# Performance work log

Hardware: AMD Instinct MI355X
Metric: run time of the kernel (lower is better)

Reference implementation:

```python
import jax, jax.numpy as jnp
import numpy as np

BN_SCALE = np.float32(1.0 / np.sqrt(1.0 + 1e-5))  # eval-mode BatchNorm: (x-0)/sqrt(1+eps)

_SPECS = {
    'x': (128, 4096, 64),
    'e_w1': (64, 64, 7),  'e_b1': (64,),
    'e_w2': (128, 64, 5), 'e_b2': (128,),
    'e_w3': (256, 128, 3),'e_b3': (256,),
    'e_w5': (256, 256, 4),'e_b5': (256,),
    'd_w1': (64, 64, 7),  'd_b1': (64,),
    'd_w2': (128, 64, 5), 'd_b2': (128,),
    'd_w3': (256, 128, 3),'d_b3': (256,),
    'd_w5': (256, 256, 4),'d_b5': (256,),
    'e_wih': (1024, 256), 'e_whh': (1024, 256), 'e_bih': (1024,), 'e_bhh': (1024,),
    'd_wih': (1024, 512), 'd_whh': (1024, 256), 'd_bih': (1024,), 'd_bhh': (1024,),
    'a_w1': (256, 512), 'a_b1': (256,), 'a_w2': (1, 256), 'a_b2': (1,),
    'f_w1': (16, 256), 'f_b1': (16,), 'f_w2': (8, 16), 'f_b2': (8,),
}

def setup_inputs() -> dict:
    key = jax.random.key(0)
    ks = jax.random.split(key, len(_SPECS))
    out = {}
    for k, (name, shape) in zip(ks, _SPECS.items()):
        scale = 1.0 if name == 'x' else 0.05
        out[name] = jax.random.normal(k, shape, dtype=jnp.float32) * scale
    return out

def _conv1d(x, w, b, pad):
    # x: (B,C,L), w: (O,I,K)
    y = jax.lax.conv_general_dilated(x, w, window_strides=(1,), padding=[(pad, pad)],
                                     dimension_numbers=('NCH', 'OIH', 'NCH'))
    return y + b[None, :, None]

def _maxpool(x, k):
    return jax.lax.reduce_window(x, -jnp.inf, jax.lax.max, (1, 1, k), (1, 1, k), 'VALID')

def _convnet(x, p):
    # faithful to the source: torch.reshape (raw reshape, NOT transpose)
    B, S, D = x.shape
    x = x.reshape(B, D, S)
    x = jax.nn.relu(_maxpool(_conv1d(x, p[0], p[1], 2), 4) * BN_SCALE)
    x = jax.nn.relu(_maxpool(_conv1d(x, p[2], p[3], 2), 4) * BN_SCALE)
    x = jax.nn.relu(_maxpool(_conv1d(x, p[4], p[5], 2), 2) * BN_SCALE)
    x = _conv1d(x, p[6], p[7], 2)
    B, C, L = x.shape
    return x.reshape(B, L, C)  # raw reshape, as in source

def _lstm_step(hs, cs, xt, wih, whh, bih, bhh):
    g = xt @ wih.T + bih + hs @ whh.T + bhh
    i, f, gg, o = jnp.split(g, 4, axis=-1)
    cs = jax.nn.sigmoid(f) * cs + jax.nn.sigmoid(i) * jnp.tanh(gg)
    hs = jax.nn.sigmoid(o) * jnp.tanh(cs)
    return hs, cs

def _forward(x, e_w1, e_b1, e_w2, e_b2, e_w3, e_b3, e_w5, e_b5,
             d_w1, d_b1, d_w2, d_b2, d_w3, d_b3, d_w5, d_b5,
             e_wih, e_whh, e_bih, e_bhh, d_wih, d_whh, d_bih, d_bhh,
             a_w1, a_b1, a_w2, a_b2, f_w1, f_b1, f_w2, f_b2):
    B = x.shape[0]
    H = e_whh.shape[1]
    enc = _convnet(x, (e_w1, e_b1, e_w2, e_b2, e_w3, e_b3, e_w5, e_b5))  # (B,T,4D)
    h0 = jnp.zeros((B, H), x.dtype)
    c0 = jnp.zeros((B, H), x.dtype)

    def enc_step(carry, xt):
        hs, cs = _lstm_step(carry[0], carry[1], xt, e_wih, e_whh, e_bih, e_bhh)
        return (hs, cs), hs
    (hs, cs), ann = jax.lax.scan(enc_step, (h0, c0), jnp.swapaxes(enc, 0, 1))
    ann = jnp.swapaxes(ann, 0, 1)  # (B,T,H)

    dec = _convnet(x, (d_w1, d_b1, d_w2, d_b2, d_w3, d_b3, d_w5, d_b5))  # (B,T,4D)

    def dec_step(carry, xt):
        hs, cs = carry
        q = jnp.broadcast_to(hs[:, None, :], ann.shape)          # (B,T,H)
        cat = jnp.concatenate([q, ann], axis=2)                  # (B,T,2H)
        u = jax.nn.relu(jnp.einsum('btk,hk->bth', cat, a_w1) + a_b1)
        u = jnp.einsum('bth,oh->bto', u, a_w2) + a_b2            # (B,T,1)
        w = jax.nn.softmax(u, axis=1)
        ctx = jnp.einsum('bto,bth->bh', w, ann)                  # (B,H)
        inp = jnp.concatenate([xt, ctx], axis=1)                 # (B,4D+H)
        hs, cs = _lstm_step(hs, cs, inp, d_wih, d_whh, d_bih, d_bhh)
        return (hs, cs), None
    (hs, cs), _ = jax.lax.scan(dec_step, (hs, cs), jnp.swapaxes(dec, 0, 1))

    y = jax.nn.relu(hs @ f_w1.T + f_b1)
    return jax.nn.sigmoid(y @ f_w2.T + f_b2)

def reference(x, e_w1, e_b1, e_w2, e_b2, e_w3, e_b3, e_w5, e_b5,
              d_w1, d_b1, d_w2, d_b2, d_w3, d_b3, d_w5, d_b5,
              e_wih, e_whh, e_bih, e_bhh, d_wih, d_whh, d_bih, d_bhh,
              a_w1, a_b1, a_w2, a_b2, f_w1, f_b1, f_w2, f_b2):
    return _forward(x, e_w1, e_b1, e_w2, e_b2, e_w3, e_b3, e_w5, e_b5,
                    d_w1, d_b1, d_w2, d_b2, d_w3, d_b3, d_w5, d_b5,
                    e_wih, e_whh, e_bih, e_bhh, d_wih, d_whh, d_bih, d_bhh,
                    a_w1, a_b1, a_w2, a_b2, f_w1, f_b1, f_w2, f_b2)
```

## Files before the change

kernel.cpp:

```cpp
#include <hip/hip_runtime.h>
#include <cmath>

#define BN_SCALE 0.9999950000374997f

__device__ __forceinline__ float sigm(float x) { return 1.f / (1.f + __expf(-x)); }

__device__ __forceinline__ void gsync(unsigned* bar, unsigned target) {
    __syncthreads();
    if (threadIdx.x == 0) {
        __threadfence();
        atomicAdd(bar, 1u);
        while (__hip_atomic_load(bar, __ATOMIC_RELAXED, __HIP_MEMORY_SCOPE_AGENT) < target)
            __builtin_amdgcn_s_sleep(2);
        __threadfence();
    }
    __syncthreads();
}

template<int I, int K, int POOL, int O4, int OPAR, int IC, bool ACT>
__global__ __launch_bounds__(256) void conv2k(
    const float* __restrict__ in, const float* __restrict__ w,
    const float* __restrict__ bias, float* __restrict__ out,
    int O, int Lin, int Lpool)
{
    constexpr int TLP = 256 / OPAR;
    constexpr int NLP = TLP * 4;
    constexpr int LC  = NLP / POOL;
    constexpr int SEG = NLP + K - 1;
    constexpr int PW  = O4 * OPAR;
    constexpr int ICH = I / IC;
    __shared__ float xs[IC * SEG];
    __shared__ float ws[PW * IC * K];

    const int chunk = blockIdx.x, b = blockIdx.y, tid = threadIdx.x;
    const int l0 = chunk * LC;
    const int jbase = chunk * NLP - 2;
    const int tlp = tid % TLP, og = tid / TLP;
    const int lp0 = tlp * 4;
    const int npass = O / PW;
    const float* inb = in + (size_t)b * I * Lin;

    for (int p = 0; p < npass; ++p) {
        float acc[O4][4];
        #pragma unroll
        for (int oo = 0; oo < O4; ++oo)
            #pragma unroll
            for (int j = 0; j < 4; ++j) acc[oo][j] = 0.f;

        for (int c = 0; c < ICH; ++c) {
            __syncthreads();
            for (int idx = tid; idx < PW * IC * K; idx += 256) {
                int oo = idx / (IC * K); int rem = idx % (IC * K);
                int ii = rem / K; int k = rem % K;
                ws[idx] = w[(size_t)((p * PW + oo) * I + c * IC + ii) * K + k];
            }
            if (ICH > 1 || p == 0) {
                for (int idx = tid; idx < IC * SEG; idx += 256) {
                    int ii = idx / SEG, s = idx % SEG;
                    int j = jbase + s;
                    float v = 0.f;
                    if (j >= 0 && j < Lin) v = inb[(size_t)(c * IC + ii) * Lin + j];
                    xs[idx] = v;
                }
            }
            __syncthreads();
            for (int ii = 0; ii < IC; ++ii) {
                float xv[K + 3];
                #pragma unroll
                for (int k = 0; k < K + 3; ++k) xv[k] = xs[ii * SEG + lp0 + k];
                #pragma unroll
                for (int oo = 0; oo < O4; ++oo) {
                    const float* wr = &ws[((og * O4 + oo) * IC + ii) * K];
                    #pragma unroll
                    for (int k = 0; k < K; ++k) {
                        float wv = wr[k];
                        acc[oo][0] += wv * xv[k];
                        acc[oo][1] += wv * xv[k + 1];
                        acc[oo][2] += wv * xv[k + 2];
                        acc[oo][3] += wv * xv[k + 3];
                    }
                }
            }
        }
        #pragma unroll
        for (int oo = 0; oo < O4; ++oo) {
            int o = p * PW + og * O4 + oo;
            float bv = bias[o];
            #pragma unroll
            for (int wnd = 0; wnd < 4 / POOL; ++wnd) {
                float m = acc[oo][wnd * POOL];
                #pragma unroll
                for (int q = 1; q < POOL; ++q) m = fmaxf(m, acc[oo][wnd * POOL + q]);
                int l = l0 + lp0 / POOL + wnd;
                if (l < Lpool) {
                    float v = m + bv;
                    if (ACT) v = fmaxf(v * BN_SCALE, 0.f);
                    out[((size_t)b * O + o) * Lpool + l] = v;
                }
            }
        }
    }
}

__global__ __launch_bounds__(256) void transpose_kt(
    const float* __restrict__ in, float* __restrict__ out, int N, int ldin, int off)
{
    int idx = blockIdx.x * 256 + threadIdx.x;
    int k = idx / N, n = idx % N;
    out[idx] = in[(size_t)n * ldin + off + k];
}

__global__ __launch_bounds__(256) void pack_aw1hs(
    const float* __restrict__ aw1, float* __restrict__ out)
{
    int idx = blockIdx.x * 256 + threadIdx.x;
    int c = idx & 3, h = (idx >> 2) & 255, k4 = idx >> 10;
    out[idx] = aw1[(size_t)h * 512 + k4 * 4 + c];
}

template<int N>
__global__ __launch_bounds__(256) void gemm16(
    const float* __restrict__ X, const float* __restrict__ WT,
    const float* __restrict__ b1, const float* __restrict__ b2,
    float* __restrict__ OUT, int outT, int outB)
{
    constexpr int NL = N / 4;
    constexpr int MS = N >> 6;
    __shared__ float xsh[16][257];
    const int m0 = blockIdx.x * 16;
    const int tt = m0 >> 7, bb0 = m0 & 127;
    const int tid = threadIdx.x;
    for (int it = 0; it < 16; ++it)
        xsh[it][tid] = X[(size_t)(bb0 + it) * 33024 + tt * 256 + tid];
    __syncthreads();
    const int mg = tid / NL, nl = tid % NL;
    float4 acc[MS];
    #pragma unroll
    for (int i = 0; i < MS; ++i) acc[i] = make_float4(0.f, 0.f, 0.f, 0.f);
    for (int k = 0; k < 256; ++k) {
        float4 wv = *(const float4*)(WT + (size_t)k * N + nl * 4);
        #pragma unroll
        for (int ms = 0; ms < MS; ++ms) {
            float s = xsh[mg * MS + ms][k];
            acc[ms].x += wv.x * s; acc[ms].y += wv.y * s;
            acc[ms].z += wv.z * s; acc[ms].w += wv.w * s;
        }
    }
    float4 bv = *(const float4*)(b1 + nl * 4);
    if (b2) {
        float4 b2v = *(const float4*)(b2 + nl * 4);
        bv.x += b2v.x; bv.y += b2v.y; bv.z += b2v.z; bv.w += b2v.w;
    }
    #pragma unroll
    for (int ms = 0; ms < MS; ++ms) {
        int mi = mg * MS + ms;
        float4 v = acc[ms];
        v.x += bv.x; v.y += bv.y; v.z += bv.z; v.w += bv.w;
        *(float4*)(OUT + (size_t)tt * outT + (size_t)(bb0 + mi) * outB + nl * 4) = v;
    }
}

__global__ __launch_bounds__(256) void enc_persist(
    const float* __restrict__ IH, const float* __restrict__ whh,
    float* __restrict__ hs0, float* __restrict__ hs1,
    float* __restrict__ cs_out, float* __restrict__ ann, unsigned* __restrict__ bar)
{
    const int blk = blockIdx.x, tid = threadIdx.x;
    const int jg = blk & 31, bg = blk >> 5;
    __shared__ float whh_sl[32 * 260];
    __shared__ float hs_l[16 * 260];
    __shared__ float g_l[16 * 33];
    for (int r = 0; r < 32; ++r) {
        int o = (r >> 3) * 256 + jg * 8 + (r & 7);
        whh_sl[r * 260 + tid] = whh[(size_t)o * 256 + tid];
    }
    float cs_r = 0.f;
    unsigned phase = 0;
    __syncthreads();
    for (int step = 0; step < 129; ++step) {
        const float* cur = (step & 1) ? hs1 : hs0;
        float* nxt = (step & 1) ? hs0 : hs1;
        for (int it = 0; it < 16; ++it)
            hs_l[it * 260 + tid] = cur[(bg * 16 + it) * 256 + tid];
        __syncthreads();
        const int bb = tid >> 4, r0 = tid & 15;
        #pragma unroll
        for (int half = 0; half < 2; ++half) {
            int r = r0 + half * 16;
            int o = (r >> 3) * 256 + jg * 8 + (r & 7);
            float a = IH[(size_t)step * 131072 + (size_t)(bg * 16 + bb) * 1024 + o];
            const float* wr = &whh_sl[r * 260];
            const float* hr = &hs_l[bb * 260];
            for (int k4 = 0; k4 < 64; ++k4) {
                float4 w4 = *(const float4*)(wr + k4 * 4);
                float4 h4 = *(const float4*)(hr + k4 * 4);
                a += w4.x * h4.x + w4.y * h4.y + w4.z * h4.z + w4.w * h4.w;
            }
            g_l[bb * 33 + r] = a;
        }
        __syncthreads();
        if (tid < 128) {
            int bb2 = tid >> 3, jj = tid & 7;
            float gi = g_l[bb2 * 33 + jj],      gf = g_l[bb2 * 33 + 8 + jj];
            float gg = g_l[bb2 * 33 + 16 + jj], go = g_l[bb2 * 33 + 24 + jj];
            float cn = sigm(gf) * cs_r + sigm(gi) * tanhf(gg);
            float hn = sigm(go) * tanhf(cn);
            cs_r = cn;
            int b = bg * 16 + bb2, j = jg * 8 + jj;
            nxt[b * 256 + j] = hn;
            ann[(size_t)b * 33024 + step * 256 + j] = hn;
            if (step == 128) cs_out[b * 256 + j] = cn;
        }
        gsync(bar, 256u * (++phase));
    }
}

__global__ __launch_bounds__(256) void dec_persist(
    const float* __restrict__ IH, const float* __restrict__ dwih,
    const float* __restrict__ dwhh, const float* __restrict__ awhs4,
    const float* __restrict__ aw2, const float* __restrict__ ann,
    const float* __restrict__ annW, float* __restrict__ ctx_g,
    float* __restrict__ hs0, float* __restrict__ hs1,
    const float* __restrict__ cs_in, unsigned* __restrict__ bar)
{
    const int blk = blockIdx.x, tid = threadIdx.x;
    const int jg = blk & 31, bg = blk >> 5;
    __shared__ float wih_sl[32 * 260];
    __shared__ float whh_sl[32 * 260];
    __shared__ float hs_l[16 * 260];
    __shared__ float ctx_l[16 * 260];
    __shared__ float g_l[16 * 33];
    __shared__ float hs_a[256], hsW_l[256], aw2_l[256], evs[256], red[256];

    for (int r = 0; r < 32; ++r) {
        int o = (r >> 3) * 256 + jg * 8 + (r & 7);
        wih_sl[r * 260 + tid] = dwih[(size_t)o * 512 + 256 + tid];
        whh_sl[r * 260 + tid] = dwhh[(size_t)o * 256 + tid];
    }
    aw2_l[tid] = aw2[tid];
    float cs_r = 0.f;
    if (tid < 128)
        cs_r = cs_in[(size_t)(bg * 16 + (tid >> 3)) * 256 + jg * 8 + (tid & 7)];
    unsigned phase = 0;
    __syncthreads();

    for (int step = 0; step < 129; ++step) {
        const float* cur = (step & 1) ? hs1 : hs0;
        float* nxt = (step & 1) ? hs0 : hs1;
        if (blk < 128) {
            hs_a[tid] = cur[blk * 256 + tid];
            __syncthreads();
            float a = 0.f;
            for (int k4 = 0; k4 < 64; ++k4) {
                float4 wv = *(const float4*)(awhs4 + (size_t)k4 * 1024 + tid * 4);
                float4 hv = *(const float4*)(&hs_a[k4 * 4]);
                a += wv.x * hv.x + wv.y * hv.y + wv.z * hv.z + wv.w * hv.w;
            }
            hsW_l[tid] = a;
            __syncthreads();
            float sv = -3.0e38f;
            if (tid < 129) {
                const float* ar = annW + (size_t)blk * 33024 + tid * 256;
                float s = 0.f;
                for (int h4 = 0; h4 < 64; ++h4) {
                    float4 av = *(const float4*)(ar + h4 * 4);
                    s += fmaxf(hsW_l[h4*4+0] + av.x, 0.f) * aw2_l[h4*4+0];
                    s += fmaxf(hsW_l[h4*4+1] + av.y, 0.f) * aw2_l[h4*4+1];
                    s += fmaxf(hsW_l[h4*4+2] + av.z, 0.f) * aw2_l[h4*4+2];
                    s += fmaxf(hsW_l[h4*4+3] + av.w, 0.f) * aw2_l[h4*4+3];
                }
                sv = s;
            }
            red[tid] = sv; __syncthreads();
            for (int s2 = 128; s2 > 0; s2 >>= 1) {
                if (tid < s2) red[tid] = fmaxf(red[tid], red[tid + s2]);
                __syncthreads();
            }
            float mx = red[0]; __syncthreads();
            float e = (tid < 129) ? __expf(sv - mx) : 0.f;
            evs[tid] = e; red[tid] = e; __syncthreads();
            for (int s2 = 128; s2 > 0; s2 >>= 1) {
                if (tid < s2) red[tid] += red[tid + s2];
                __syncthreads();
            }
            float inv = 1.f / red[0];
            float c = 0.f;
            const float* ab = ann + (size_t)blk * 33024 + tid;
            for (int t2 = 0; t2 < 129; ++t2) c += evs[t2] * ab[(size_t)t2 * 256];
            ctx_g[blk * 256 + tid] = c * inv;
        }
        gsync(bar, 256u * (++phase));
        for (int it = 0; it < 16; ++it) {
            hs_l[it * 260 + tid]  = cur[(bg * 16 + it) * 256 + tid];
            ctx_l[it * 260 + tid] = ctx_g[(bg * 16 + it) * 256 + tid];
        }
        __syncthreads();
        {
            const int bb = tid >> 4, r0 = tid & 15;
            const float* hr = &hs_l[bb * 260];
            const float* cr = &ctx_l[bb * 260];
            #pragma unroll
            for (int half = 0; half < 2; ++half) {
                int r = r0 + half * 16;
                int o = (r >> 3) * 256 + jg * 8 + (r & 7);
                float a = IH[(size_t)step * 131072 + (size_t)(bg * 16 + bb) * 1024 + o];
                const float* w1 = &wih_sl[r * 260];
                const float* w2 = &whh_sl[r * 260];
                for (int k4 = 0; k4 < 64; ++k4) {
                    float4 u  = *(const float4*)(w1 + k4 * 4);
                    float4 cv = *(const float4*)(cr + k4 * 4);
                    float4 v  = *(const float4*)(w2 + k4 * 4);
                    float4 hv = *(const float4*)(hr + k4 * 4);
                    a += u.x * cv.x + u.y * cv.y + u.z * cv.z + u.w * cv.w;
                    a += v.x * hv.x + v.y * hv.y + v.z * hv.z + v.w * hv.w;
                }
                g_l[bb * 33 + r] = a;
            }
        }
        __syncthreads();
        if (tid < 128) {
            int bb2 = tid >> 3, jj = tid & 7;
            float gi = g_l[bb2 * 33 + jj],      gf = g_l[bb2 * 33 + 8 + jj];
            float gg = g_l[bb2 * 33 + 16 + jj], go = g_l[bb2 * 33 + 24 + jj];
            float cn = sigm(gf) * cs_r + sigm(gi) * tanhf(gg);
            float hn = sigm(go) * tanhf(cn);
            cs_r = cn;
            nxt[(bg * 16 + bb2) * 256 + jg * 8 + jj] = hn;
        }
        gsync(bar, 256u * (++phase));
    }
}

__global__ __launch_bounds__(256) void final_kernel(
    const float* __restrict__ hs,
    const float* __restrict__ fw1, const float* __restrict__ fb1,
    const float* __restrict__ fw2, const float* __restrict__ fb2,
    float* __restrict__ out)
{
    const int b = blockIdx.x, t = threadIdx.x;
    __shared__ float hsh[256], ysh[16];
    hsh[t] = hs[(size_t)b * 256 + t];
    __syncthreads();
    if (t < 16) {
        float a = fb1[t];
        const float* wr = fw1 + (size_t)t * 256;
        for (int k = 0; k < 256; ++k) a += wr[k] * hsh[k];
        ysh[t] = fmaxf(a, 0.f);
    }
    __syncthreads();
    if (t < 8) {
        float a = fb2[t];
        const float* wr = fw2 + (size_t)t * 16;
        for (int k = 0; k < 16; ++k) a += wr[k] * ysh[k];
        out[(size_t)b * 8 + t] = 1.f / (1.f + __expf(-a));
    }
}

extern "C" void kernel_launch(void* const* d_in, const int* in_sizes, int n_in,
                              void* d_out, int out_size, void* d_ws, size_t ws_size,
                              hipStream_t stream)
{
    const float* x     = (const float*)d_in[0];
    const float* e_w1  = (const float*)d_in[1];
    const float* e_b1  = (const float*)d_in[2];
    const float* e_w2  = (const float*)d_in[3];
    const float* e_b2  = (const float*)d_in[4];
    const float* e_w3  = (const float*)d_in[5];
    const float* e_b3  = (const float*)d_in[6];
    const float* e_w5  = (const float*)d_in[7];
    const float* e_b5  = (const float*)d_in[8];
    const float* d_w1  = (const float*)d_in[9];
    const float* d_b1  = (const float*)d_in[10];
    const float* d_w2  = (const float*)d_in[11];
    const float* d_b2  = (const float*)d_in[12];
    const float* d_w3  = (const float*)d_in[13];
    const float* d_b3  = (const float*)d_in[14];
    const float* d_w5  = (const float*)d_in[15];
    const float* d_b5  = (const float*)d_in[16];
    const float* e_wih = (const float*)d_in[17];
    const float* e_whh = (const float*)d_in[18];
    const float* e_bih = (const float*)d_in[19];
    const float* e_bhh = (const float*)d_in[20];
    const float* d_wih = (const float*)d_in[21];
    const float* d_whh = (const float*)d_in[22];
    const float* d_bih = (const float*)d_in[23];
    const float* d_bhh = (const float*)d_in[24];
    const float* a_w1  = (const float*)d_in[25];
    const float* a_b1  = (const float*)d_in[26];
    const float* a_w2  = (const float*)d_in[27];
    const float* f_w1  = (const float*)d_in[29];
    const float* f_b1  = (const float*)d_in[30];
    const float* f_w2  = (const float*)d_in[31];
    const float* f_b2  = (const float*)d_in[32];

    float* ws = (float*)d_ws;
    float* enc_feat = ws;
    float* dec_feat = ws + 4227072;
    float* IH       = ws + 8454144;
    float* conv_reg = ws + 25362432;
    float* hsA      = ws + 42115072;
    float* hsB      = ws + 42147840;
    float* cs_g     = ws + 42180608;

    float* pool1 = conv_reg;
    float* pool2 = conv_reg + 8380416;
    float* pool3 = conv_reg + 12558336;
    float* ann      = conv_reg;
    float* annW     = conv_reg + 4227072;
    float* e_wihT   = conv_reg + 8454144;
    float* d_wihT   = conv_reg + 8716288;
    float* aw1T_ann = conv_reg + 8978432;
    float* aw1T_hs4 = conv_reg + 9043968;
    float* ctx_g    = conv_reg + 9109504;
    unsigned* bars  = (unsigned*)(conv_reg + 9142272);

    dim3 blk(256);

    conv2k< 64, 7, 4, 2, 8, 64, true ><<<dim3(32, 128), blk, 0, stream>>>(x,     e_w1, e_b1, pool1,     64, 4096, 1023);
    conv2k< 64, 5, 4, 2, 8, 64, true ><<<dim3( 8, 128), blk, 0, stream>>>(pool1, e_w2, e_b2, pool2,    128, 1023,  255);
    conv2k<128, 3, 2, 2, 8, 64, true ><<<dim3( 2, 128), blk, 0, stream>>>(pool2, e_w3, e_b3, pool3,    256,  255,  128);
    conv2k<256, 4, 1, 2, 8, 64, false><<<dim3( 2, 128), blk, 0, stream>>>(pool3, e_w5, e_b5, enc_feat, 256,  128,  129);
    conv2k< 64, 7, 4, 2, 8, 64, true ><<<dim3(32, 128), blk, 0, stream>>>(x,     d_w1, d_b1, pool1,     64, 4096, 1023);
    conv2k< 64, 5, 4, 2, 8, 64, true ><<<dim3( 8, 128), blk, 0, stream>>>(pool1, d_w2, d_b2, pool2,    128, 1023,  255);
    conv2k<128, 3, 2, 2, 8, 64, true ><<<dim3( 2, 128), blk, 0, stream>>>(pool2, d_w3, d_b3, pool3,    256,  255,  128);
    conv2k<256, 4, 1, 2, 8, 64, false><<<dim3( 2, 128), blk, 0, stream>>>(pool3, d_w5, d_b5, dec_feat, 256,  128,  129);

    hipMemsetAsync(hsA, 0, 131072, stream);
    hipMemsetAsync(bars, 0, 256, stream);

    transpose_kt<<<dim3(1024), blk, 0, stream>>>(e_wih, e_wihT, 1024, 256, 0);
    transpose_kt<<<dim3(1024), blk, 0, stream>>>(d_wih, d_wihT, 1024, 512, 0);
    transpose_kt<<<dim3( 256), blk, 0, stream>>>(a_w1, aw1T_ann, 256, 512, 256);
    pack_aw1hs  <<<dim3( 256), blk, 0, stream>>>(a_w1, aw1T_hs4);

    gemm16<1024><<<dim3(1032), blk, 0, stream>>>(enc_feat, e_wihT, e_bih, e_bhh, IH, 131072, 1024);
    enc_persist<<<dim3(256), blk, 0, stream>>>(IH, e_whh, hsA, hsB, cs_g, ann, bars);

    gemm16< 256><<<dim3(1032), blk, 0, stream>>>(ann, aw1T_ann, a_b1, nullptr, annW, 256, 33024);
    gemm16<1024><<<dim3(1032), blk, 0, stream>>>(dec_feat, d_wihT, d_bih, d_bhh, IH, 131072, 1024);

    dec_persist<<<dim3(256), blk, 0, stream>>>(IH, d_wih, d_whh, aw1T_hs4, a_w2,
                                               ann, annW, ctx_g, hsB, hsA, cs_g, bars + 32);

    final_kernel<<<dim3(128), blk, 0, stream>>>(hsA, f_w1, f_b1, f_w2, f_b2, (float*)d_out);

    (void)in_sizes; (void)n_in; (void)out_size; (void)ws_size;
}
```

Before: 19.01 ms.

## Replace grid-synchronized persistent LSTM kernels with per-batch 1024-thread blocks

The encoder and decoder recurrences no longer use 256-block persistent kernels with atomic grid barriers every step. Each of 128 blocks now owns one batch element and computes all 1024 gates locally, so the only per-step synchronisation is __syncthreads. The attention, softmax and context steps move inside the same block, and the final MLP is fused into the decoder kernel. In exchange, each thread streams its recurrent weight rows from global/L2 every step instead of keeping them in shared memory, and only 128 workgroups run.

After: 18.79 ms. About the same (-1.1%).

```diff
diff --git a/kernel.cpp b/kernel.cpp
--- a/kernel.cpp
+++ b/kernel.cpp
@@ -4,18 +4,6 @@
 #define BN_SCALE 0.9999950000374997f
 
 __device__ __forceinline__ float sigm(float x) { return 1.f / (1.f + __expf(-x)); }
-
-__device__ __forceinline__ void gsync(unsigned* bar, unsigned target) {
-    __syncthreads();
-    if (threadIdx.x == 0) {
-        __threadfence();
-        atomicAdd(bar, 1u);
-        while (__hip_atomic_load(bar, __ATOMIC_RELAXED, __HIP_MEMORY_SCOPE_AGENT) < target)
-            __builtin_amdgcn_s_sleep(2);
-        __threadfence();
-    }
-    __syncthreads();
-}
 
 template<int I, int K, int POOL, int O4, int OPAR, int IC, bool ACT>
 __global__ __launch_bounds__(256) void conv2k(
@@ -108,14 +96,6 @@
     int idx = blockIdx.x * 256 + threadIdx.x;
     int k = idx / N, n = idx % N;
     out[idx] = in[(size_t)n * ldin + off + k];
-}
-
-__global__ __launch_bounds__(256) void pack_aw1hs(
-    const float* __restrict__ aw1, float* __restrict__ out)
-{
-    int idx = blockIdx.x * 256 + threadIdx.x;
-    int c = idx & 3, h = (idx >> 2) & 255, k4 = idx >> 10;
-    out[idx] = aw1[(size_t)h * 512 + k4 * 4 + c];
 }
 
 template<int N>
@@ -160,199 +140,172 @@
     }
 }
 
-__global__ __launch_bounds__(256) void enc_persist(
+__global__ __launch_bounds__(1024) void enc_batch(
     const float* __restrict__ IH, const float* __restrict__ whh,
-    float* __restrict__ hs0, float* __restrict__ hs1,
-    float* __restrict__ cs_out, float* __restrict__ ann, unsigned* __restrict__ bar)
-{
-    const int blk = blockIdx.x, tid = threadIdx.x;
-    const int jg = blk & 31, bg = blk >> 5;
-    __shared__ float whh_sl[32 * 260];
-    __shared__ float hs_l[16 * 260];
-    __shared__ float g_l[16 * 33];
-    for (int r = 0; r < 32; ++r) {
-        int o = (r >> 3) * 256 + jg * 8 + (r & 7);
-        whh_sl[r * 260 + tid] = whh[(size_t)o * 256 + tid];
-    }
+    float* __restrict__ ann, float* __restrict__ hs_out, float* __restrict__ cs_out)
+{
+    const int b = blockIdx.x, tid = threadIdx.x;
+    __shared__ float hs_l[256];
+    __shared__ float g_l[1024];
+    if (tid < 256) hs_l[tid] = 0.f;
     float cs_r = 0.f;
-    unsigned phase = 0;
+    const float4* wr = (const float4*)(whh + (size_t)tid * 256);
     __syncthreads();
-    for (int step = 0; step < 129; ++step) {
-        const float* cur = (step & 1) ? hs1 : hs0;
-        float* nxt = (step & 1) ? hs0 : hs1;
-        for (int it = 0; it < 16; ++it)
-            hs_l[it * 260 + tid] = cur[(bg * 16 + it) * 256 + tid];
-        __syncthreads();
-        const int bb = tid >> 4, r0 = tid & 15;
-        #pragma unroll
-        for (int half = 0; half < 2; ++half) {
-            int r = r0 + half * 16;
-            int o = (r >> 3) * 256 + jg * 8 + (r & 7);
-            float a = IH[(size_t)step * 131072 + (size_t)(bg * 16 + bb) * 1024 + o];
-            const float* wr = &whh_sl[r * 260];
-            const float* hr = &hs_l[bb * 260];
-            for (int k4 = 0; k4 < 64; ++k4) {
-                float4 w4 = *(const float4*)(wr + k4 * 4);
-                float4 h4 = *(const float4*)(hr + k4 * 4);
-                a += w4.x * h4.x + w4.y * h4.y + w4.z * h4.z + w4.w * h4.w;
-            }
-            g_l[bb * 33 + r] = a;
-        }
-        __syncthreads();
-        if (tid < 128) {
-            int bb2 = tid >> 3, jj = tid & 7;
-            float gi = g_l[bb2 * 33 + jj],      gf = g_l[bb2 * 33 + 8 + jj];
-            float gg = g_l[bb2 * 33 + 16 + jj], go = g_l[bb2 * 33 + 24 + jj];
+    for (int t = 0; t < 129; ++t) {
+        float a = IH[(size_t)t * 131072 + b * 1024 + tid];
+        for (int k4 = 0; k4 < 64; ++k4) {
+            float4 w4 = wr[k4];
+            float4 h4 = *(const float4*)(&hs_l[k4 * 4]);
+            a += w4.x * h4.x + w4.y * h4.y + w4.z * h4.z + w4.w * h4.w;
+        }
+        g_l[tid] = a;
+        __syncthreads();
+        if (tid < 256) {
+            float gi = g_l[tid],       gf = g_l[256 + tid];
+            float gg = g_l[512 + tid], go = g_l[768 + tid];
             float cn = sigm(gf) * cs_r + sigm(gi) * tanhf(gg);
             float hn = sigm(go) * tanhf(cn);
             cs_r = cn;
-            int b = bg * 16 + bb2, j = jg * 8 + jj;
-            nxt[b * 256 + j] = hn;
-            ann[(size_t)b * 33024 + step * 256 + j] = hn;
-            if (step == 128) cs_out[b * 256 + j] = cn;
-        }
-        gsync(bar, 256u * (++phase));
-    }
-}
-
-__global__ __launch_bounds__(256) void dec_persist(
+            hs_l[tid] = hn;
+            ann[(size_t)b * 33024 + t * 256 + tid] = hn;
+            if (t == 128) { hs_out[b * 256 + tid] = hn; cs_out[b * 256 + tid] = cn; }
+        }
+        __syncthreads();
+    }
+}
+
+__global__ __launch_bounds__(1024) void dec_batch(
     const float* __restrict__ IH, const float* __restrict__ dwih,
-    const float* __restrict__ dwhh, const float* __restrict__ awhs4,
+    const float* __restrict__ dwhh, const float* __restrict__ aw1,
     const float* __restrict__ aw2, const float* __restrict__ ann,
-    const float* __restrict__ annW, float* __restrict__ ctx_g,
-    float* __restrict__ hs0, float* __restrict__ hs1,
-    const float* __restrict__ cs_in, unsigned* __restrict__ bar)
-{
-    const int blk = blockIdx.x, tid = threadIdx.x;
-    const int jg = blk & 31, bg = blk >> 5;
-    __shared__ float wih_sl[32 * 260];
-    __shared__ float whh_sl[32 * 260];
-    __shared__ float hs_l[16 * 260];
-    __shared__ float ctx_l[16 * 260];
-    __shared__ float g_l[16 * 33];
-    __shared__ float hs_a[256], hsW_l[256], aw2_l[256], evs[256], red[256];
-
-    for (int r = 0; r < 32; ++r) {
-        int o = (r >> 3) * 256 + jg * 8 + (r & 7);
-        wih_sl[r * 260 + tid] = dwih[(size_t)o * 512 + 256 + tid];
-        whh_sl[r * 260 + tid] = dwhh[(size_t)o * 256 + tid];
-    }
-    aw2_l[tid] = aw2[tid];
-    float cs_r = 0.f;
-    if (tid < 128)
-        cs_r = cs_in[(size_t)(bg * 16 + (tid >> 3)) * 256 + jg * 8 + (tid & 7)];
-    unsigned phase = 0;
+    const float* __restrict__ annW,
+    const float* __restrict__ hs_in, const float* __restrict__ cs_in,
+    const float* __restrict__ fw1, const float* __restrict__ fb1,
+    const float* __restrict__ fw2, const float* __restrict__ fb2,
+    float* __restrict__ out)
+{
+    const int b = blockIdx.x, tid = threadIdx.x;
+    __shared__ float hs_l[256], ctx_l[256], hsW_l[256], aw2_l[256];
+    __shared__ float g_l[1024], part[1024];
+    __shared__ float ev_l[256], sred[256], ssum[256];
+    __shared__ float inv_l;
+    __shared__ float ysh[16];
+
+    if (tid < 256) { hs_l[tid] = hs_in[b * 256 + tid]; aw2_l[tid] = aw2[tid]; }
+    float cs_r = (tid < 256) ? cs_in[b * 256 + tid] : 0.f;
+
+    const int hq = tid >> 2, qc = tid & 3;
+    const float4* awr = (const float4*)(aw1 + (size_t)hq * 512 + qc * 64);
+    const float4* u4 = (const float4*)(dwih + (size_t)tid * 512 + 256);
+    const float4* v4 = (const float4*)(dwhh + (size_t)tid * 256);
     __syncthreads();
 
-    for (int step = 0; step < 129; ++step) {
-        const float* cur = (step & 1) ? hs1 : hs0;
-        float* nxt = (step & 1) ? hs0 : hs1;
-        if (blk < 128) {
-            hs_a[tid] = cur[blk * 256 + tid];
-            __syncthreads();
+    for (int t = 0; t < 129; ++t) {
+        {
             float a = 0.f;
+            #pragma unroll
+            for (int k4 = 0; k4 < 16; ++k4) {
+                float4 w4 = awr[k4];
+                float4 h4 = *(const float4*)(&hs_l[qc * 64 + k4 * 4]);
+                a += w4.x * h4.x + w4.y * h4.y + w4.z * h4.z + w4.w * h4.w;
+            }
+            part[tid] = a;
+        }
+        __syncthreads();
+        if (tid < 256)
+            hsW_l[tid] = part[tid * 4] + part[tid * 4 + 1] + part[tid * 4 + 2] + part[tid * 4 + 3];
+        __syncthreads();
+
+        if (tid < 516) {
+            int tt = tid >> 2, c = tid & 3;
+            const float4* ar = (const float4*)(annW + (size_t)b * 33024 + tt * 256 + c * 64);
+            float s = 0.f;
+            #pragma unroll
+            for (int k4 = 0; k4 < 16; ++k4) {
+                float4 av = ar[k4];
+                int k = c * 64 + k4 * 4;
+                s += fmaxf(hsW_l[k]     + av.x, 0.f) * aw2_l[k]
+                   + fmaxf(hsW_l[k + 1] + av.y, 0.f) * aw2_l[k + 1]
+                   + fmaxf(hsW_l[k + 2] + av.z, 0.f) * aw2_l[k + 2]
+                   + fmaxf(hsW_l[k + 3] + av.w, 0.f) * aw2_l[k + 3];
+            }
+            part[tid] = s;
+        }
+        __syncthreads();
+        float sv = -3.0e38f;
+        if (tid < 129)
+            sv = part[tid * 4] + part[tid * 4 + 1] + part[tid * 4 + 2] + part[tid * 4 + 3];
+        if (tid < 256) sred[tid] = sv;
+        __syncthreads();
+        if (tid < 64) {
+            float m = fmaxf(fmaxf(sred[tid], sred[tid + 64]),
+                            fmaxf(sred[tid + 128], sred[tid + 192]));
+            #pragma unroll
+            for (int d = 32; d > 0; d >>= 1) m = fmaxf(m, __shfl_xor(m, d));
+            if (tid == 0) sred[0] = m;
+        }
+        __syncthreads();
+        const float mx = sred[0];
+        float e = (tid < 129) ? __expf(sv - mx) : 0.f;
+        if (tid < 256) { ev_l[tid] = e; ssum[tid] = e; }
+        __syncthreads();
+        if (tid < 64) {
+            float s = ssum[tid] + ssum[tid + 64] + ssum[tid + 128] + ssum[tid + 192];
+            #pragma unroll
+            for (int d = 32; d > 0; d >>= 1) s += __shfl_xor(s, d);
+            if (tid == 0) inv_l = 1.f / s;
+        }
+        __syncthreads();
+
+        {
+            int j = tid & 255, q = tid >> 8;
+            int t0 = q * 33, t1 = t0 + 33 < 129 ? t0 + 33 : 129;
+            const float* ab = ann + (size_t)b * 33024 + j;
+            float a = 0.f;
+            for (int t2 = t0; t2 < t1; ++t2) a += ev_l[t2] * ab[(size_t)t2 * 256];
+            part[q * 256 + j] = a;
+        }
+        __syncthreads();
+        if (tid < 256)
+            ctx_l[tid] = (part[tid] + part[256 + tid] + part[512 + tid] + part[768 + tid]) * inv_l;
+        __syncthreads();
+
+        {
+            float a = IH[(size_t)t * 131072 + b * 1024 + tid];
             for (int k4 = 0; k4 < 64; ++k4) {
-                float4 wv = *(const float4*)(awhs4 + (size_t)k4 * 1024 + tid * 4);
-                float4 hv = *(const float4*)(&hs_a[k4 * 4]);
-                a += wv.x * hv.x + wv.y * hv.y + wv.z * hv.z + wv.w * hv.w;
-            }
-            hsW_l[tid] = a;
-            __syncthreads();
-            float sv = -3.0e38f;
-            if (tid < 129) {
-                const float* ar = annW + (size_t)blk * 33024 + tid * 256;
-                float s = 0.f;
-                for (int h4 = 0; h4 < 64; ++h4) {
-                    float4 av = *(const float4*)(ar + h4 * 4);
-                    s += fmaxf(hsW_l[h4*4+0] + av.x, 0.f) * aw2_l[h4*4+0];
-                    s += fmaxf(hsW_l[h4*4+1] + av.y, 0.f) * aw2_l[h4*4+1];
-                    s += fmaxf(hsW_l[h4*4+2] + av.z, 0.f) * aw2_l[h4*4+2];
-                    s += fmaxf(hsW_l[h4*4+3] + av.w, 0.f) * aw2_l[h4*4+3];
-                }
-                sv = s;
-            }
-            red[tid] = sv; __syncthreads();
-            for (int s2 = 128; s2 > 0; s2 >>= 1) {
-                if (tid < s2) red[tid] = fmaxf(red[tid], red[tid + s2]);
-                __syncthreads();
-            }
-            float mx = red[0]; __syncthreads();
-            float e = (tid < 129) ? __expf(sv - mx) : 0.f;
-            evs[tid] = e; red[tid] = e; __syncthreads();
-            for (int s2 = 128; s2 > 0; s2 >>= 1) {
-                if (tid < s2) red[tid] += red[tid + s2];
-                __syncthreads();
-            }
-            float inv = 1.f / red[0];
-            float c = 0.f;
-            const float* ab = ann + (size_t)blk * 33024 + tid;
-            for (int t2 = 0; t2 < 129; ++t2) c += evs[t2] * ab[(size_t)t2 * 256];
-            ctx_g[blk * 256 + tid] = c * inv;
-        }
-        gsync(bar, 256u * (++phase));
-        for (int it = 0; it < 16; ++it) {
-            hs_l[it * 260 + tid]  = cur[(bg * 16 + it) * 256 + tid];
-            ctx_l[it * 260 + tid] = ctx_g[(bg * 16 + it) * 256 + tid];
-        }
-        __syncthreads();
-        {
-            const int bb = tid >> 4, r0 = tid & 15;
-            const float* hr = &hs_l[bb * 260];
-            const float* cr = &ctx_l[bb * 260];
-            #pragma unroll
-            for (int half = 0; half < 2; ++half) {
-                int r = r0 + half * 16;
-                int o = (r >> 3) * 256 + jg * 8 + (r & 7);
-                float a = IH[(size_t)step * 131072 + (size_t)(bg * 16 + bb) * 1024 + o];
-                const float* w1 = &wih_sl[r * 260];
-                const float* w2 = &whh_sl[r * 260];
-                for (int k4 = 0; k4 < 64; ++k4) {
-                    float4 u  = *(const float4*)(w1 + k4 * 4);
-                    float4 cv = *(const float4*)(cr + k4 * 4);
-                    float4 v  = *(const float4*)(w2 + k4 * 4);
-                    float4 hv = *(const float4*)(hr + k4 * 4);
-                    a += u.x * cv.x + u.y * cv.y + u.z * cv.z + u.w * cv.w;
-                    a += v.x * hv.x + v.y * hv.y + v.z * hv.z + v.w * hv.w;
-                }
-                g_l[bb * 33 + r] = a;
-            }
-        }
-        __syncthreads();
-        if (tid < 128) {
-            int bb2 = tid >> 3, jj = tid & 7;
-            float gi = g_l[bb2 * 33 + jj],      gf = g_l[bb2 * 33 + 8 + jj];
-            float gg = g_l[bb2 * 33 + 16 + jj], go = g_l[bb2 * 33 + 24 + jj];
+                float4 u  = u4[k4];
+                float4 cv = *(const float4*)(&ctx_l[k4 * 4]);
+                float4 v  = v4[k4];
+                float4 hv = *(const float4*)(&hs_l[k4 * 4]);
+                a += u.x * cv.x + u.y * cv.y + u.z * cv.z + u.w * cv.w;
+                a += v.x * hv.x + v.y * hv.y + v.z * hv.z + v.w * hv.w;
+            }
+            g_l[tid] = a;
+        }
+        __syncthreads();
+        if (tid < 256) {
+            float gi = g_l[tid],       gf = g_l[256 + tid];
+            float gg = g_l[512 + tid], go = g_l[768 + tid];
             float cn = sigm(gf) * cs_r + sigm(gi) * tanhf(gg);
             float hn = sigm(go) * tanhf(cn);
             cs_r = cn;
-            nxt[(bg * 16 + bb2) * 256 + jg * 8 + jj] = hn;
-        }
-        gsync(bar, 256u * (++phase));
-    }
-}
-
-__global__ __launch_bounds__(256) void final_kernel(
-    const float* __restrict__ hs,
-    const float* __restrict__ fw1, const float* __restrict__ fb1,
-    const float* __restrict__ fw2, const float* __restrict__ fb2,
-    float* __restrict__ out)
-{
-    const int b = blockIdx.x, t = threadIdx.x;
-    __shared__ float hsh[256], ysh[16];
-    hsh[t] = hs[(size_t)b * 256 + t];
+            hs_l[tid] = hn;
+        }
+        __syncthreads();
+    }
+
+    if (tid < 16) {
+        float a = fb1[tid];
+        const float* wr = fw1 + (size_t)tid * 256;
+        for (int k = 0; k < 256; ++k) a += wr[k] * hs_l[k];
+        ysh[tid] = fmaxf(a, 0.f);
+    }
     __syncthreads();
-    if (t < 16) {
-        float a = fb1[t];
-        const float* wr = fw1 + (size_t)t * 256;
-        for (int k = 0; k < 256; ++k) a += wr[k] * hsh[k];
-        ysh[t] = fmaxf(a, 0.f);
-    }
-    __syncthreads();
-    if (t < 8) {
-        float a = fb2[t];
-        const float* wr = fw2 + (size_t)t * 16;
+    if (tid < 8) {
+        float a = fb2[tid];
+        const float* wr = fw2 + (size_t)tid * 16;
         for (int k = 0; k < 16; ++k) a += wr[k] * ysh[k];
-        out[(size_t)b * 8 + t] = 1.f / (1.f + __expf(-a));
+        out[(size_t)b * 8 + tid] = 1.f / (1.f + __expf(-a));
     }
 }
 
@@ -399,8 +352,7 @@
     float* IH       = ws + 8454144;
     float* conv_reg = ws + 25362432;
     float* hsA      = ws + 42115072;
-    float* hsB      = ws + 42147840;
-    float* cs_g     = ws + 42180608;
+    float* cs_g     = ws + 42147840;
 
     float* pool1 = conv_reg;
     float* pool2 = conv_reg + 8380416;
@@ -410,9 +362,6 @@
     float* e_wihT   = conv_reg + 8454144;
     float* d_wihT   = conv_reg + 8716288;
     float* aw1T_ann = conv_reg + 8978432;
-    float* aw1T_hs4 = conv_reg + 9043968;
-    float* ctx_g    = conv_reg + 9109504;
-    unsigned* bars  = (unsigned*)(conv_reg + 9142272);
 
     dim3 blk(256);
 
@@ -425,24 +374,18 @@
     conv2k<128, 3, 2, 2, 8, 64, true ><<<dim3( 2, 128), blk, 0, stream>>>(pool2, d_w3, d_b3, pool3,    256,  255,  128);
     conv2k<256, 4, 1, 2, 8, 64, false><<<dim3( 2, 128), blk, 0, stream>>>(pool3, d_w5, d_b5, dec_feat, 256,  128,  129);
 
-    hipMemsetAsync(hsA, 0, 131072, stream);
-    hipMemsetAsync(bars, 0, 256, stream);
-
     transpose_kt<<<dim3(1024), blk, 0, stream>>>(e_wih, e_wihT, 1024, 256, 0);
     transpose_kt<<<dim3(1024), blk, 0, stream>>>(d_wih, d_wihT, 1024, 512, 0);
     transpose_kt<<<dim3( 256), blk, 0, stream>>>(a_w1, aw1T_ann, 256, 512, 256);
-    pack_aw1hs  <<<dim3( 256), blk, 0, stream>>>(a_w1, aw1T_hs4);
 
     gemm16<1024><<<dim3(1032), blk, 0, stream>>>(enc_feat, e_wihT, e_bih, e_bhh, IH, 131072, 1024);
-    enc_persist<<<dim3(256), blk, 0, stream>>>(IH, e_whh, hsA, hsB, cs_g, ann, bars);
+    enc_batch<<<dim3(128), dim3(1024), 0, stream>>>(IH, e_whh, ann, hsA, cs_g);
 
     gemm16< 256><<<dim3(1032), blk, 0, stream>>>(ann, aw1T_ann, a_b1, nullptr, annW, 256, 33024);
     gemm16<1024><<<dim3(1032), blk, 0, stream>>>(dec_feat, d_wihT, d_bih, d_bhh, IH, 131072, 1024);
 
-    dec_persist<<<dim3(256), blk, 0, stream>>>(IH, d_wih, d_whh, aw1T_hs4, a_w2,
-                                               ann, annW, ctx_g, hsB, hsA, cs_g, bars + 32);
-
-    final_kernel<<<dim3(128), blk, 0, stream>>>(hsA, f_w1, f_b1, f_w2, f_b2, (float*)d_out);
+    dec_batch<<<dim3(128), dim3(1024), 0, stream>>>(IH, d_wih, d_whh, a_w1, a_w2,
+        ann, annW, hsA, cs_g, f_w1, f_b1, f_w2, f_b2, (float*)d_out);
 
     (void)in_sizes; (void)n_in; (void)out_size; (void)ws_size;
 }
```
